# Performance work log

Measured on AMD Instinct MI355X. Metric: run time of the kernel, lower is better.

## Reference

```python
import jax, jax.numpy as jnp
import numpy as np

CODEBOOK_SIZE = 4096
EMBED_DIM = 256
BETA = 0.25


def setup_inputs() -> dict:
    key = jax.random.key(0)
    k_z, k_cb = jax.random.split(key)
    z = jax.random.normal(k_z, (32, 256, 32, 32), dtype=jnp.float32)
    # nn.Embedding weight init: uniform(-1/D, 1/D)
    codebook = jax.random.uniform(
        k_cb, (CODEBOOK_SIZE, EMBED_DIM), dtype=jnp.float32,
        minval=-1.0 / EMBED_DIM, maxval=1.0 / EMBED_DIM)
    return {"z": z, "codebook": codebook}


def reference(z, codebook):
    b, c, h, w = z.shape
    # (B,C,H,W) -> (B*H*W, D)
    z_flat = jnp.transpose(z, (0, 2, 3, 1)).reshape(-1, c)
    # squared euclidean distances: ||z||^2 - 2 z.e^T + ||e||^2  (== cdist(...)^2)
    z_sq = jnp.sum(z_flat * z_flat, axis=1, keepdims=True)          # (N,1)
    e_sq = jnp.sum(codebook * codebook, axis=1)                     # (K,)
    distances = z_sq - 2.0 * (z_flat @ codebook.T) + e_sq[None, :]  # (N,K)
    min_encoding_indices = jnp.argmin(distances, axis=1)            # (N,)
    z_q_flat = codebook[min_encoding_indices]                       # (N,D)
    z_q = jnp.transpose(z_q_flat.reshape(b, h, w, c), (0, 3, 1, 2))  # (B,C,H,W)
    # straight-through estimator
    z_q_st = z + jax.lax.stop_gradient(z_q - z)
    codebook_loss = jnp.mean((z_q - jax.lax.stop_gradient(z)) ** 2)
    commitment_loss = jnp.mean((z - jax.lax.stop_gradient(z_q)) ** 2)
    vq_loss = codebook_loss + BETA * commitment_loss
    return (z_q_st, vq_loss, min_encoding_indices.reshape(b, h, w))
```

## Files before the change

kernel.cpp:

```cpp
#include <hip/hip_runtime.h>

#define K_CODES 4096
#define D 256
#define N_VEC 32768
#define N_ELEM 8388608
#define WINDOW 3.5e-4f
#define WINDOW_C 5.25e-4f
#define CAP 14
#define CSTRIDE 16
#define RG 8
#define RSLICE 256

typedef _Float16 f16x8 __attribute__((ext_vector_type(8)));
typedef float f32x4 __attribute__((ext_vector_type(4)));

#define WS_LOSS 0
#define WS_COUNT 8
#define WS_DONE 16
#define WS_COUNT2 24
#define WS_IDX 256
#define WS_LIST (WS_IDX + N_VEC * 4)
#define WS_ESQ (WS_LIST + N_VEC * 4)
#define WS_ZSQ (WS_ESQ + K_CODES * 4)
#define WS_APACK (WS_ZSQ + N_VEC * 4)
#define WS_BPACK (WS_APACK + (size_t)N_VEC * 256 * 2)
#define WS_RFIN (WS_BPACK + (size_t)K_CODES * 256 * 2 + 65536)
#define WS_ZT (WS_RFIN + (size_t)N_VEC * 8)
#define WS_NEED_ZT (WS_ZT + (size_t)N_VEC * D * 4)
#define WS_S1F WS_NEED_ZT
#define WS_CANDN (WS_S1F + (size_t)N_VEC * 4)
#define WS_CANDL (WS_CANDN + (size_t)N_VEC * 4)
#define WS_LISTB (WS_CANDL + (size_t)N_VEC * CSTRIDE * 2)
#define WS_NEED_CAND (WS_LISTB + (size_t)N_VEC * 4)

#define PREP_PZ 4096
#define PREP_PCB 512
#define PREP_ESQ 1024
#define PREP_ZSQ 128
#define PREP_BLOCKS (PREP_PZ + PREP_PCB + PREP_ESQ + PREP_ZSQ)

__device__ __forceinline__ unsigned long long pack_key(float s, int idx) {
  const unsigned u = __float_as_uint(s);
  const unsigned mk = (u & 0x80000000u) ? ~u : (u | 0x80000000u);
  return ((unsigned long long)mk << 12) | (unsigned long long)(unsigned)idx;
}
__device__ __forceinline__ float key_score(unsigned long long k) {
  const unsigned mk = (unsigned)(k >> 12);
  const unsigned u = (mk & 0x80000000u) ? (mk & 0x7fffffffu) : ~mk;
  return __uint_as_float(u);
}

__device__ __forceinline__ void pin_frag(f16x8& v) {
  asm volatile("" : "+v"(v));
}

__device__ void esq_body(int bx, const float* __restrict__ cb,
                         float* __restrict__ esq) {
  const int lane = threadIdx.x & 63;
  const int k = bx * 4 + (threadIdx.x >> 6);
  const float* row = cb + (size_t)k * D;
  double s = 0.;
#pragma unroll
  for (int j = 0; j < 4; ++j) {
    const float v = row[lane + 64 * j];
    s += (double)__fmul_rn(v, v);
  }
#pragma unroll
  for (int off = 32; off > 0; off >>= 1) s += __shfl_down(s, off, 64);
  if (lane == 0) esq[k] = (float)s;
}

__device__ void zsq_body(int bx, const float* __restrict__ z,
                         float* __restrict__ zsq) {
  const int n = bx * 256 + threadIdx.x;
  const int b = n >> 10;
  const int hw = n & 1023;
  const float* p = z + ((size_t)b << 18) + hw;
  double a0 = 0., a1 = 0., a2 = 0., a3 = 0.;
  for (int c = 0; c < D; c += 4) {
    const float v0 = p[(size_t)(c + 0) << 10];
    const float v1 = p[(size_t)(c + 1) << 10];
    const float v2 = p[(size_t)(c + 2) << 10];
    const float v3 = p[(size_t)(c + 3) << 10];
    a0 += (double)__fmul_rn(v0, v0);
    a1 += (double)__fmul_rn(v1, v1);
    a2 += (double)__fmul_rn(v2, v2);
    a3 += (double)__fmul_rn(v3, v3);
  }
  zsq[n] = (float)((a0 + a1) + (a2 + a3));
}

__device__ void pack_z2_body(int bx, const float* __restrict__ z,
                             _Float16* __restrict__ Ap,
                             float* __restrict__ zT) {
  const int t = bx * 256 + threadIdx.x;
  const int lane = t & 63;
  const int fid = t >> 6;
  const int ks = fid & 7;
  const int grp = fid >> 3;
  const int n = grp * 16 + (lane & 15);
  const int d = ks * 32 + ((lane >> 4) << 3);
  const int b = n >> 10, hw = n & 1023;
  const float* p = z + ((size_t)b << 18) + ((size_t)d << 10) + hw;
  float v[8];
  f16x8 H;
#pragma unroll
  for (int j = 0; j < 8; ++j) {
    v[j] = p[(size_t)j << 10];
    H[j] = (_Float16)v[j];
  }
  *(f16x8*)(Ap + (size_t)t * 8) = H;
  if (zT) {
    float4* o = (float4*)(zT + (size_t)n * D + d);
    o[0] = make_float4(v[0], v[1], v[2], v[3]);
    o[1] = make_float4(v[4], v[5], v[6], v[7]);
  }
}

__device__ void pack_cb2_body(int bx, const float* __restrict__ cb,
                              _Float16* __restrict__ Bp) {
  const int t = bx * 256 + threadIdx.x;
  const int lane = t & 63;
  const int fid = t >> 6;
  const int ks = fid & 7;
  const int grp = fid >> 3;
  const int k = grp * 16 + (lane & 15);
  const int d = ks * 32 + ((lane >> 4) << 3);
  const float* p = cb + (size_t)k * D + d;
  f16x8 H;
#pragma unroll
  for (int j = 0; j < 8; ++j) H[j] = (_Float16)(p[j] * 256.f);
  *(f16x8*)(Bp + (size_t)t * 8) = H;
}

__global__ __launch_bounds__(256) void prep_kernel(
    const float* __restrict__ z, const float* __restrict__ cb,
    float* __restrict__ esq, float* __restrict__ zsq,
    _Float16* __restrict__ Ap, _Float16* __restrict__ Bp,
    float* __restrict__ zT) {
  const int b = blockIdx.x;
  if (b < PREP_PZ) {
    pack_z2_body(b, z, Ap, zT);
  } else if (b < PREP_PZ + PREP_PCB) {
    pack_cb2_body(b - PREP_PZ, cb, Bp);
  } else if (b < PREP_PZ + PREP_PCB + PREP_ESQ) {
    esq_body(b - PREP_PZ - PREP_PCB, cb, esq);
  } else {
    zsq_body(b - PREP_PZ - PREP_PCB - PREP_ESQ, z, zsq);
  }
}

__global__ __launch_bounds__(512, 2) void dist2_kernel(
    const _Float16* __restrict__ Ap, const _Float16* __restrict__ Bp,
    const float* __restrict__ esq, int* __restrict__ idx,
    int* __restrict__ list, unsigned int* __restrict__ count,
    unsigned long long* __restrict__ rfin, float* __restrict__ s1f,
    int* __restrict__ listB, unsigned int* __restrict__ count2) {
  __shared__ unsigned long long mb[128][4][2];
  const int tid = threadIdx.x;
  const int lane = tid & 63;
  const int w = tid >> 6;
  const int wn = w >> 2;
  const int wc = w & 3;
  const int n0 = blockIdx.x * 128;

  f16x8 a[4][8];
  {
    const _Float16* ab =
        Ap + (size_t)((n0 + wn * 64) >> 4) * 4096 + (size_t)lane * 8;
#pragma unroll
    for (int ni = 0; ni < 4; ++ni)
#pragma unroll
      for (int ks = 0; ks < 8; ++ks) {
        a[ni][ks] = *(const f16x8*)(ab + (size_t)(ni * 8 + ks) * 512);
        pin_frag(a[ni][ks]);
      }
  }

  float s1[4], s2[4];
  int i1[4];
#pragma unroll
  for (int ni = 0; ni < 4; ++ni) {
    s1[ni] = 3.4e38f;
    s2[ni] = 3.4e38f;
    i1[ni] = 0;
  }

  const _Float16* bbase = Bp + (size_t)wc * 4096 + (size_t)lane * 8;
  const int crow = wc * 16 + ((lane >> 4) << 2);
  const f32x4 z4 = (f32x4)0.f;

  f16x8 b[8];
#pragma unroll
  for (int ks = 0; ks < 8; ++ks)
    b[ks] = *(const f16x8*)(bbase + (size_t)ks * 512);

  for (int t = 0; t < 64; ++t) {
    const float4 e4 = *(const float4*)(esq + t * 64 + crow);
    f32x4 acc0, acc1, acc2, acc3;
    __builtin_amdgcn_s_setprio(1);
#pragma unroll
    for (int ks = 0; ks < 8; ++ks) {
      acc0 = __builtin_amdgcn_mfma_f32_16x16x32_f16(b[ks], a[0][ks],
                                                    ks ? acc0 : z4, 0, 0, 0);
      acc1 = __builtin_amdgcn_mfma_f32_16x16x32_f16(b[ks], a[1][ks],
                                                    ks ? acc1 : z4, 0, 0, 0);
      acc2 = __builtin_amdgcn_mfma_f32_16x16x32_f16(b[ks], a[2][ks],
                                                    ks ? acc2 : z4, 0, 0, 0);
      acc3 = __builtin_amdgcn_mfma_f32_16x16x32_f16(b[ks], a[3][ks],
                                                    ks ? acc3 : z4, 0, 0, 0);
      b[ks] = *(const f16x8*)(bbase + (size_t)(t + 1) * 16384 + ks * 512);
    }
    __builtin_amdgcn_s_setprio(0);
    const int cb0 = t * 64 + crow;
    const float ev[4] = {e4.x, e4.y, e4.z, e4.w};
    f32x4 accv[4] = {acc0, acc1, acc2, acc3};
#pragma unroll
    for (int r = 0; r < 4; ++r) {
      const int code = cb0 + r;
#pragma unroll
      for (int ni = 0; ni < 4; ++ni) {
        const float s = fmaf(accv[ni][r], -0.0078125f, ev[r]);
        s2[ni] = fminf(fmaxf(s, s1[ni]), s2[ni]);
        if (s < s1[ni]) i1[ni] = code;
        s1[ni] = fminf(s1[ni], s);
      }
    }
  }

  unsigned long long k1[4], k2[4];
#pragma unroll
  for (int ni = 0; ni < 4; ++ni) {
    float a1 = s1[ni], a2 = s2[ni];
    int ai1 = i1[ni];
#pragma unroll
    for (int m = 16; m <= 32; m <<= 1) {
      const float bv1 = __shfl_xor(a1, m, 64);
      const int bi1 = __shfl_xor(ai1, m, 64);
      const float bv2 = __shfl_xor(a2, m, 64);
      const float hi = fmaxf(a1, bv1);
      const bool take = (bv1 < a1) || (bv1 == a1 && bi1 < ai1);
      if (take) ai1 = bi1;
      a1 = fminf(a1, bv1);
      a2 = fminf(fminf(a2, bv2), hi);
    }
    k1[ni] = pack_key(a1, ai1);
    k2[ni] = pack_key(a2, 0);
  }
  if (lane < 16) {
#pragma unroll
    for (int ni = 0; ni < 4; ++ni) {
      const int nl = wn * 64 + ni * 16 + lane;
      mb[nl][wc][0] = k1[ni];
      mb[nl][wc][1] = k2[ni];
    }
  }
  __syncthreads();
  if (tid < 128) {
    unsigned long long m1 = ~0ull, m2 = ~0ull;
#pragma unroll
    for (int s = 0; s < 4; ++s) {
      const unsigned long long c1 = mb[tid][s][0];
      const unsigned long long c2 = mb[tid][s][1];
      if (c1 < m1) {
        m2 = m1;
        m1 = c1;
      } else if (c1 < m2) {
        m2 = c1;
      }
      if (c2 < m2) m2 = c2;
    }
    const int n = n0 + tid;
    idx[n] = (int)(m1 & 0xFFFULL);
    const float sc0 = key_score(m1);
    if (s1f) s1f[n] = sc0;
    const bool flag = key_score(m2) - sc0 < WINDOW;
    rfin[n] = flag ? ~0ull : 0ull;
    if (flag) {
      if (s1f) {
        const unsigned pos = atomicAdd(count, 1u);
        if (pos < N_VEC) list[pos] = n;
      } else {
        const unsigned p2 = atomicAdd(count2, 1u);
        if (p2 < N_VEC) listB[p2] = n;
      }
    }
  }
}

__global__ __launch_bounds__(256) void certify_kernel(
    const _Float16* __restrict__ Ap, const _Float16* __restrict__ Bp,
    const float* __restrict__ esq, const float* __restrict__ s1f,
    const int* __restrict__ list, const unsigned int* __restrict__ count,
    unsigned int* __restrict__ candn, unsigned short* __restrict__ candl,
    int* __restrict__ listB, unsigned int* __restrict__ count2) {
  if (!candn) return;
  __shared__ unsigned int lcnt[32];
  __shared__ unsigned int lcodes[32][CAP];
  unsigned int cN = *count;
  if (cN > N_VEC) cN = N_VEC;
  if (cN == 0) return;
  const int tid = threadIdx.x;
  const int lane = tid & 63;
  const int wc = tid >> 6;
  const int l16 = lane & 15;
  const int quad = lane >> 4;
  const unsigned tiles = (cN + 31) / 32;
  const f32x4 z4 = (f32x4)0.f;
  for (unsigned tile = blockIdx.x; tile < tiles; tile += gridDim.x) {
    __syncthreads();
    if (tid < 32) lcnt[tid] = 0;
    __syncthreads();
    float thrv[2];
    f16x8 af[2][8];
#pragma unroll
    for (int ni = 0; ni < 2; ++ni) {
      unsigned r = tile * 32 + ni * 16 + l16;
      if (r >= cN) r = cN - 1;
      const int n = list[r];
      thrv[ni] = s1f[n] + WINDOW_C;
      const _Float16* ab = Ap + (size_t)(n >> 4) * 4096 +
                           (size_t)quad * 128 + (size_t)(n & 15) * 8;
#pragma unroll
      for (int ks = 0; ks < 8; ++ks) {
        af[ni][ks] = *(const f16x8*)(ab + (size_t)ks * 512);
        pin_frag(af[ni][ks]);
      }
    }
    const _Float16* bbase = Bp + (size_t)wc * 4096 + (size_t)lane * 8;
    for (int t = 0; t < 64; ++t) {
      const int cb0 = t * 64 + wc * 16 + quad * 4;
      const float4 e4 = *(const float4*)(esq + cb0);
      f16x8 bf[8];
#pragma unroll
      for (int ks = 0; ks < 8; ++ks)
        bf[ks] = *(const f16x8*)(bbase + (size_t)t * 16384 + ks * 512);
      f32x4 acc0, acc1;
#pragma unroll
      for (int ks = 0; ks < 8; ++ks) {
        acc0 = __builtin_amdgcn_mfma_f32_16x16x32_f16(bf[ks], af[0][ks],
                                                      ks ? acc0 : z4, 0, 0, 0);
        acc1 = __builtin_amdgcn_mfma_f32_16x16x32_f16(bf[ks], af[1][ks],
                                                      ks ? acc1 : z4, 0, 0, 0);
      }
      const float ev[4] = {e4.x, e4.y, e4.z, e4.w};
#pragma unroll
      for (int r = 0; r < 4; ++r) {
        const float sA = fmaf(acc0[r], -0.0078125f, ev[r]);
        const float sB = fmaf(acc1[r], -0.0078125f, ev[r]);
        if (sA < thrv[0]) {
          const unsigned u = atomicAdd(&lcnt[l16], 1u);
          if (u < CAP) lcodes[l16][u] = (unsigned)(cb0 + r);
        }
        if (sB < thrv[1]) {
          const unsigned u = atomicAdd(&lcnt[16 + l16], 1u);
          if (u < CAP) lcodes[16 + l16][u] = (unsigned)(cb0 + r);
        }
      }
    }
    __syncthreads();
    if (tid < 32) {
      const unsigned r = tile * 32 + tid;
      if (r < cN) {
        const int n = list[r];
        const unsigned c = lcnt[tid];
        if (c <= CAP) {
          candn[n] = c;
          for (unsigned u = 0; u < c; ++u)
            candl[(size_t)n * CSTRIDE + u] = (unsigned short)lcodes[tid][u];
        } else {
          candn[n] = 0xFFFFFFFFu;
          const unsigned p = atomicAdd(count2, 1u);
          if (p < N_VEC) listB[p] = n;
        }
      }
    }
  }
}

__global__ __launch_bounds__(256) void rescanB_kernel(
    const float* __restrict__ zT, const float* __restrict__ cb,
    const float* __restrict__ esq, const float* __restrict__ zsq,
    const int* __restrict__ list, const unsigned int* __restrict__ count,
    const unsigned int* __restrict__ candn,
    const unsigned short* __restrict__ candl,
    unsigned long long* __restrict__ rfin) {
  if (!candn) return;
  unsigned int cN = *count;
  if (cN > N_VEC) cN = N_VEC;
  const int tid = threadIdx.x;
  const int j8 = tid & 7;
  for (unsigned i = blockIdx.x * 32 + (tid >> 3); i < cN;
       i += gridDim.x * 32) {
    const int n = list[i];
    const unsigned c = candn[n];
    if (c > CAP) continue;
    unsigned long long best = ~0ull;
    for (unsigned jj = j8; jj < c; jj += 8) {
      const int k = candl[(size_t)n * CSTRIDE + jj];
      const float* zr = zT + (size_t)n * D;
      const float* row = cb + (size_t)k * D;
      double a = 0.;
      for (int cc = 0; cc < D; cc += 4) {
        const float4 zf = *(const float4*)(zr + cc);
        const float4 r4 = *(const float4*)(row + cc);
        a = fma((double)zf.x, (double)r4.x, a);
        a = fma((double)zf.y, (double)r4.y, a);
        a = fma((double)zf.z, (double)r4.z, a);
        a = fma((double)zf.w, (double)r4.w, a);
      }
      const float d =
          __fadd_rn(__fsub_rn(zsq[n], __fmul_rn(2.0f, (float)a)), esq[k]);
      best = min(best, pack_key(d, k));
    }
    best = min(best, __shfl_xor(best, 1, 64));
    best = min(best, __shfl_xor(best, 2, 64));
    best = min(best, __shfl_xor(best, 4, 64));
    if (j8 == 0) atomicMin(rfin + n, best);
  }
}

__global__ __launch_bounds__(256) void rescan_kernel(
    const float* __restrict__ z, const float* __restrict__ zT,
    const float* __restrict__ cb, const float* __restrict__ esq,
    const float* __restrict__ zsq, const int* __restrict__ list,
    const unsigned int* __restrict__ count,
    unsigned long long* __restrict__ rfin) {
  __shared__ double zrow[RG][D];
  __shared__ int nloc[RG];
  __shared__ float zsv[RG];
  const int tid = threadIdx.x;
  const int lane = tid & 63;
  unsigned int cnt = *count;
  if (cnt > N_VEC) cnt = N_VEC;
  const unsigned G = (cnt + RG - 1) / RG;
  const unsigned nitems = G * (K_CODES / RSLICE);
  for (unsigned item = blockIdx.x; item < nitems; item += gridDim.x) {
    const unsigned g = item >> 4;
    const int s = item & 15;
    __syncthreads();
    if (tid < RG) {
      const unsigned r = g * RG + tid;
      const int n = (r < cnt) ? list[r] : list[cnt - 1];
      nloc[tid] = n;
      zsv[tid] = zsq[n];
    }
    __syncthreads();
    if (zT) {
      for (int i = tid; i < RG * D; i += 256) {
        const int p = i >> 8, c = i & 255;
        zrow[p][c] = (double)zT[(size_t)nloc[p] * D + c];
      }
    } else {
      for (int i = tid; i < RG * D; i += 256) {
        const int p = i >> 8, c = i & 255;
        const int n = nloc[p];
        const int b = n >> 10, hw = n & 1023;
        zrow[p][c] = (double)z[((size_t)b << 18) + ((size_t)c << 10) + hw];
      }
    }
    __syncthreads();
    const int k = s * RSLICE + tid;
    const float* row = cb + (size_t)k * D;
    double acc[RG];
#pragma unroll
    for (int p = 0; p < RG; ++p) acc[p] = 0.;
    for (int c = 0; c < D; c += 4) {
      const float4 r4 = *(const float4*)(row + c);
      const double rx = (double)r4.x, ry = (double)r4.y;
      const double rz = (double)r4.z, rw = (double)r4.w;
#pragma unroll
      for (int p = 0; p < RG; ++p) {
        const double2 za = *(const double2*)&zrow[p][c];
        const double2 zb = *(const double2*)&zrow[p][c + 2];
        double a = acc[p];
        a = fma(za.x, rx, a);
        a = fma(za.y, ry, a);
        a = fma(zb.x, rz, a);
        a = fma(zb.y, rw, a);
        acc[p] = a;
      }
    }
    const float ek = esq[k];
    unsigned long long best[RG];
#pragma unroll
    for (int p = 0; p < RG; ++p) {
      const float dotf = (float)acc[p];
      const float d = __fadd_rn(__fsub_rn(zsv[p], __fmul_rn(2.0f, dotf)), ek);
      best[p] = pack_key(d, k);
    }
#pragma unroll
    for (int p = 0; p < RG; ++p) {
#pragma unroll
      for (int off = 32; off > 0; off >>= 1)
        best[p] = min(best[p], __shfl_down(best[p], off, 64));
    }
    if (lane == 0) {
#pragma unroll
      for (int p = 0; p < RG; ++p) atomicMin(rfin + nloc[p], best[p]);
    }
  }
}

__global__ __launch_bounds__(256) void gather_kernel(
    const float* __restrict__ z, const float* __restrict__ cb,
    const int* __restrict__ idxarr, const unsigned long long* __restrict__ rfin,
    float* __restrict__ out, float* __restrict__ loss_acc,
    unsigned int* __restrict__ done) {
  const int tid = threadIdx.x;
  const int n0 = blockIdx.x * 64;
  const int hwl = tid & 63;
  const int cq = tid >> 6;
  const int n = n0 + hwl;
  const int b = n >> 10;
  const int hw = n & 1023;
  const unsigned long long rf = rfin[n];
  const int idx = rf ? (int)(rf & 0xFFFULL) : idxarr[n];
  if (tid < 64) out[(size_t)N_ELEM + 1 + n] = (float)idx;
  const float* crow = cb + (size_t)idx * D;
  const size_t obase = ((size_t)b << 18) + hw;
  float part = 0.f;
#pragma unroll
  for (int j = 0; j < 16; ++j) {
    const int c = cq * 64 + j * 4;
    const float4 v4 = *(const float4*)(crow + c);
    const size_t o = obase + ((size_t)c << 10);
    const float d0 = v4.x - z[o];
    const float d1 = v4.y - z[o + 1024];
    const float d2 = v4.z - z[o + 2048];
    const float d3 = v4.w - z[o + 3072];
    out[o] = v4.x;
    out[o + 1024] = v4.y;
    out[o + 2048] = v4.z;
    out[o + 3072] = v4.w;
    part = fmaf(d0, d0, part);
    part = fmaf(d1, d1, part);
    part = fmaf(d2, d2, part);
    part = fmaf(d3, d3, part);
  }
#pragma unroll
  for (int off = 32; off > 0; off >>= 1) part += __shfl_down(part, off, 64);
  __shared__ float red[4];
  if ((tid & 63) == 0) red[tid >> 6] = part;
  __syncthreads();
  if (tid == 0) {
    atomicAdd(loss_acc, red[0] + red[1] + red[2] + red[3]);
    __threadfence();
    const unsigned old = atomicAdd(done, 1u);
    if (old == gridDim.x - 1) {
      const float total = atomicAdd(loss_acc, 0.0f);
      out[N_ELEM] = 1.25f * total * (1.0f / (float)N_ELEM);
    }
  }
}

extern "C" void kernel_launch(void* const* d_in, const int* in_sizes, int n_in,
                              void* d_out, int out_size, void* d_ws,
                              size_t ws_size, hipStream_t stream) {
  const float* z = (const float*)d_in[0];
  const float* cb = (const float*)d_in[1];
  float* out = (float*)d_out;
  char* ws = (char*)d_ws;
  float* loss_acc = (float*)(ws + WS_LOSS);
  unsigned int* count = (unsigned int*)(ws + WS_COUNT);
  unsigned int* done = (unsigned int*)(ws + WS_DONE);
  unsigned int* count2 = (unsigned int*)(ws + WS_COUNT2);
  int* idx = (int*)(ws + WS_IDX);
  int* list = (int*)(ws + WS_LIST);
  float* esq = (float*)(ws + WS_ESQ);
  float* zsq = (float*)(ws + WS_ZSQ);
  _Float16* Ap = (_Float16*)(ws + WS_APACK);
  _Float16* Bp = (_Float16*)(ws + WS_BPACK);
  unsigned long long* rfin = (unsigned long long*)(ws + WS_RFIN);
  float* zT = (ws_size >= WS_NEED_ZT) ? (float*)(ws + WS_ZT) : nullptr;
  const bool canduse = (ws_size >= WS_NEED_CAND) && (zT != nullptr);
  float* s1f = canduse ? (float*)(ws + WS_S1F) : nullptr;
  unsigned int* candn = canduse ? (unsigned int*)(ws + WS_CANDN) : nullptr;
  unsigned short* candl = canduse ? (unsigned short*)(ws + WS_CANDL) : nullptr;
  int* listB = canduse ? (int*)(ws + WS_LISTB) : list;

  hipMemsetAsync(ws, 0, 256, stream);
  prep_kernel<<<PREP_BLOCKS, 256, 0, stream>>>(z, cb, esq, zsq, Ap, Bp, zT);
  dist2_kernel<<<N_VEC / 128, 512, 0, stream>>>(Ap, Bp, esq, idx, list, count,
                                                rfin, s1f, listB, count2);
  certify_kernel<<<128, 256, 0, stream>>>(Ap, Bp, esq, s1f, list, count, candn,
                                          candl, listB, count2);
  rescanB_kernel<<<256, 256, 0, stream>>>(zT, cb, esq, zsq, list, count, candn,
                                          candl, rfin);
  rescan_kernel<<<2048, 256, 0, stream>>>(z, zT, cb, esq, zsq, listB, count2,
                                          rfin);
  gather_kernel<<<N_VEC / 64, 256, 0, stream>>>(z, cb, idx, rfin, out,
                                                loss_acc, done);
}
```

Before: 298.2 us.

## Split certify work across codebook slices with global atomic candidate lists

The certify kernel is restructured so that each 64-thread block handles one 16-vector tile against one of 16 codebook slices, replacing 256-thread blocks that each scanned the whole codebook for 32 vectors. Candidates are appended through global atomics on candn, which is now zeroed by an extra memset, instead of shared-memory lists. Overflow detection and listB queuing move into rescanB. The aim is more parallelism and better load balance when the flagged list is short, at the cost of reloading A fragments for every slice and contended global atomics.

Result: faster. 249.0 us (-16.5%).

```diff
diff --git a/kernel.cpp b/kernel.cpp
--- a/kernel.cpp
+++ b/kernel.cpp
@@ -288,90 +288,60 @@
   }
 }
 
-__global__ __launch_bounds__(256) void certify_kernel(
+__global__ __launch_bounds__(64) void certify_kernel(
     const _Float16* __restrict__ Ap, const _Float16* __restrict__ Bp,
     const float* __restrict__ esq, const float* __restrict__ s1f,
     const int* __restrict__ list, const unsigned int* __restrict__ count,
-    unsigned int* __restrict__ candn, unsigned short* __restrict__ candl,
-    int* __restrict__ listB, unsigned int* __restrict__ count2) {
+    unsigned int* __restrict__ candn, unsigned short* __restrict__ candl) {
   if (!candn) return;
-  __shared__ unsigned int lcnt[32];
-  __shared__ unsigned int lcodes[32][CAP];
   unsigned int cN = *count;
   if (cN > N_VEC) cN = N_VEC;
   if (cN == 0) return;
-  const int tid = threadIdx.x;
-  const int lane = tid & 63;
-  const int wc = tid >> 6;
+  const int lane = threadIdx.x & 63;
   const int l16 = lane & 15;
   const int quad = lane >> 4;
-  const unsigned tiles = (cN + 31) / 32;
+  const unsigned ptiles = (cN + 15) / 16;
+  const unsigned items = ptiles * 16;
   const f32x4 z4 = (f32x4)0.f;
-  for (unsigned tile = blockIdx.x; tile < tiles; tile += gridDim.x) {
-    __syncthreads();
-    if (tid < 32) lcnt[tid] = 0;
-    __syncthreads();
-    float thrv[2];
-    f16x8 af[2][8];
-#pragma unroll
-    for (int ni = 0; ni < 2; ++ni) {
-      unsigned r = tile * 32 + ni * 16 + l16;
-      if (r >= cN) r = cN - 1;
-      const int n = list[r];
-      thrv[ni] = s1f[n] + WINDOW_C;
-      const _Float16* ab = Ap + (size_t)(n >> 4) * 4096 +
-                           (size_t)quad * 128 + (size_t)(n & 15) * 8;
-#pragma unroll
-      for (int ks = 0; ks < 8; ++ks) {
-        af[ni][ks] = *(const f16x8*)(ab + (size_t)ks * 512);
-        pin_frag(af[ni][ks]);
-      }
-    }
-    const _Float16* bbase = Bp + (size_t)wc * 4096 + (size_t)lane * 8;
-    for (int t = 0; t < 64; ++t) {
-      const int cb0 = t * 64 + wc * 16 + quad * 4;
+  for (unsigned item = blockIdx.x; item < items; item += gridDim.x) {
+    const unsigned pt = item >> 4;
+    const unsigned sl = item & 15;
+    unsigned r = pt * 16 + l16;
+    const bool valid = (r < cN);
+    if (!valid) r = cN - 1;
+    const int n = list[r];
+    const float thr = s1f[n] + WINDOW_C;
+    f16x8 af[8];
+    const _Float16* ab = Ap + (size_t)(n >> 4) * 4096 + (size_t)quad * 128 +
+                         (size_t)(n & 15) * 8;
+#pragma unroll
+    for (int ks = 0; ks < 8; ++ks) {
+      af[ks] = *(const f16x8*)(ab + (size_t)ks * 512);
+      pin_frag(af[ks]);
+    }
+#pragma unroll 2
+    for (int g = 0; g < 16; ++g) {
+      const int grp = sl * 16 + g;
+      const _Float16* bb = Bp + (size_t)grp * 4096 + (size_t)lane * 8;
+      f16x8 bf[8];
+#pragma unroll
+      for (int ks = 0; ks < 8; ++ks)
+        bf[ks] = *(const f16x8*)(bb + (size_t)ks * 512);
+      f32x4 acc;
+#pragma unroll
+      for (int ks = 0; ks < 8; ++ks)
+        acc = __builtin_amdgcn_mfma_f32_16x16x32_f16(bf[ks], af[ks],
+                                                     ks ? acc : z4, 0, 0, 0);
+      const int cb0 = grp * 16 + quad * 4;
       const float4 e4 = *(const float4*)(esq + cb0);
-      f16x8 bf[8];
-#pragma unroll
-      for (int ks = 0; ks < 8; ++ks)
-        bf[ks] = *(const f16x8*)(bbase + (size_t)t * 16384 + ks * 512);
-      f32x4 acc0, acc1;
-#pragma unroll
-      for (int ks = 0; ks < 8; ++ks) {
-        acc0 = __builtin_amdgcn_mfma_f32_16x16x32_f16(bf[ks], af[0][ks],
-                                                      ks ? acc0 : z4, 0, 0, 0);
-        acc1 = __builtin_amdgcn_mfma_f32_16x16x32_f16(bf[ks], af[1][ks],
-                                                      ks ? acc1 : z4, 0, 0, 0);
-      }
       const float ev[4] = {e4.x, e4.y, e4.z, e4.w};
 #pragma unroll
-      for (int r = 0; r < 4; ++r) {
-        const float sA = fmaf(acc0[r], -0.0078125f, ev[r]);
-        const float sB = fmaf(acc1[r], -0.0078125f, ev[r]);
-        if (sA < thrv[0]) {
-          const unsigned u = atomicAdd(&lcnt[l16], 1u);
-          if (u < CAP) lcodes[l16][u] = (unsigned)(cb0 + r);
-        }
-        if (sB < thrv[1]) {
-          const unsigned u = atomicAdd(&lcnt[16 + l16], 1u);
-          if (u < CAP) lcodes[16 + l16][u] = (unsigned)(cb0 + r);
-        }
-      }
-    }
-    __syncthreads();
-    if (tid < 32) {
-      const unsigned r = tile * 32 + tid;
-      if (r < cN) {
-        const int n = list[r];
-        const unsigned c = lcnt[tid];
-        if (c <= CAP) {
-          candn[n] = c;
-          for (unsigned u = 0; u < c; ++u)
-            candl[(size_t)n * CSTRIDE + u] = (unsigned short)lcodes[tid][u];
-        } else {
-          candn[n] = 0xFFFFFFFFu;
-          const unsigned p = atomicAdd(count2, 1u);
-          if (p < N_VEC) listB[p] = n;
+      for (int rr = 0; rr < 4; ++rr) {
+        const float s = fmaf(acc[rr], -0.0078125f, ev[rr]);
+        if (valid && s < thr) {
+          const unsigned u = atomicAdd(&candn[n], 1u);
+          if (u < CAP)
+            candl[(size_t)n * CSTRIDE + u] = (unsigned short)(cb0 + rr);
         }
       }
     }
@@ -384,7 +354,8 @@
     const int* __restrict__ list, const unsigned int* __restrict__ count,
     const unsigned int* __restrict__ candn,
     const unsigned short* __restrict__ candl,
-    unsigned long long* __restrict__ rfin) {
+    unsigned long long* __restrict__ rfin, int* __restrict__ listB,
+    unsigned int* __restrict__ count2) {
   if (!candn) return;
   unsigned int cN = *count;
   if (cN > N_VEC) cN = N_VEC;
@@ -394,7 +365,13 @@
        i += gridDim.x * 32) {
     const int n = list[i];
     const unsigned c = candn[n];
-    if (c > CAP) continue;
+    if (c > CAP) {
+      if (j8 == 0) {
+        const unsigned p = atomicAdd(count2, 1u);
+        if (p < N_VEC) listB[p] = n;
+      }
+      continue;
+    }
     unsigned long long best = ~0ull;
     for (unsigned jj = j8; jj < c; jj += 8) {
       const int k = candl[(size_t)n * CSTRIDE + jj];
@@ -416,7 +393,7 @@
     best = min(best, __shfl_xor(best, 1, 64));
     best = min(best, __shfl_xor(best, 2, 64));
     best = min(best, __shfl_xor(best, 4, 64));
-    if (j8 == 0) atomicMin(rfin + n, best);
+    if (j8 == 0 && best != ~0ull) atomicMin(rfin + n, best);
   }
 }
 
@@ -580,13 +557,14 @@
   int* listB = canduse ? (int*)(ws + WS_LISTB) : list;
 
   hipMemsetAsync(ws, 0, 256, stream);
+  if (canduse) hipMemsetAsync(ws + WS_CANDN, 0, (size_t)N_VEC * 4, stream);
   prep_kernel<<<PREP_BLOCKS, 256, 0, stream>>>(z, cb, esq, zsq, Ap, Bp, zT);
   dist2_kernel<<<N_VEC / 128, 512, 0, stream>>>(Ap, Bp, esq, idx, list, count,
                                                 rfin, s1f, listB, count2);
-  certify_kernel<<<128, 256, 0, stream>>>(Ap, Bp, esq, s1f, list, count, candn,
-                                          candl, listB, count2);
+  certify_kernel<<<2048, 64, 0, stream>>>(Ap, Bp, esq, s1f, list, count, candn,
+                                          candl);
   rescanB_kernel<<<256, 256, 0, stream>>>(zT, cb, esq, zsq, list, count, candn,
-                                          candl, rfin);
+                                          candl, rfin, listB, count2);
   rescan_kernel<<<2048, 256, 0, stream>>>(z, zT, cb, esq, zsq, listB, count2,
                                           rfin);
   gather_kernel<<<N_VEC / 64, 256, 0, stream>>>(z, cb, idx, rfin, out,
```
